# Kernel optimization log

Measured on AMD Instinct MI355X. Metric: run time of the kernel, lower is better.

Reference implementation:

```python
import jax, jax.numpy as jnp
import numpy as np

T, B = 1024, 64
IN, HID, OUT, ASZ = 512, 512, 512, 128


def lstm_cell(x, h, c, Wih, Whh, bih, bhh):
    g = x @ Wih.T + bih + h @ Whh.T + bhh
    i, f, gg, o = jnp.split(g, 4, axis=1)
    c2 = jax.nn.sigmoid(f) * c + jax.nn.sigmoid(i) * jnp.tanh(gg)
    h2 = jax.nn.sigmoid(o) * jnp.tanh(c2)
    return h2, c2


def arnn_cell(x, h, pol, Wih, Whh, b, ninp, nhid):
    # policy chunks: [ninp, nhid, nhid, nhid, nhid, nhid]
    p_in = pol[:, :ninp]
    p_h = pol[:, ninp:ninp + nhid]
    p_ig = pol[:, ninp + nhid:ninp + 2 * nhid]
    p_hg = pol[:, ninp + 2 * nhid:ninp + 3 * nhid]
    p_b = pol[:, ninp + 3 * nhid:ninp + 4 * nhid]
    ig = ((x * p_in) @ Wih.T) * p_ig + b * p_b
    hg = ((h * p_h) @ Whh.T) * p_hg
    return jnp.tanh(ig + hg)


def setup_inputs() -> dict:
    key = jax.random.key(0)
    ks = list(jax.random.split(key, 24))
    s = 0.1
    d = {"x": jax.random.normal(ks[0], (T, B, IN), dtype=jnp.float32)}
    # layer 0: ninp=IN, nhid=HID; layer 1: ninp=HID, nhid=OUT
    for l, (ninp, nhid) in enumerate([(IN, HID), (HID, OUT)]):
        ain = ASZ + ninp + nhid
        psz = ninp + 5 * nhid
        base = 1 + 9 * l
        d[f"aW_ih{l}"] = jax.random.normal(ks[base + 0], (4 * ASZ, ain)) * s
        d[f"aW_hh{l}"] = jax.random.normal(ks[base + 1], (4 * ASZ, ASZ)) * s
        d[f"ab_ih{l}"] = jax.random.normal(ks[base + 2], (4 * ASZ,)) * s
        d[f"ab_hh{l}"] = jax.random.normal(ks[base + 3], (4 * ASZ,)) * s
        d[f"pW{l}"] = jax.random.normal(ks[base + 4], (psz, ASZ)) * s
        d[f"pb{l}"] = jax.random.normal(ks[base + 5], (psz,)) * s
        d[f"fW_ih{l}"] = jax.random.normal(ks[base + 6], (nhid, ninp)) * s
        d[f"fW_hh{l}"] = jax.random.normal(ks[base + 7], (nhid, nhid)) * s
        d[f"fb{l}"] = jax.random.normal(ks[base + 8], (nhid,)) * s
    return d


def reference(x, aW_ih0, aW_hh0, ab_ih0, ab_hh0, pW0, pb0, fW_ih0, fW_hh0, fb0,
              aW_ih1, aW_hh1, ab_ih1, ab_hh1, pW1, pb1, fW_ih1, fW_hh1, fb1):
    zB = lambda n: jnp.zeros((B, n), dtype=x.dtype)
    init = (zB(ASZ), zB(ASZ), zB(ASZ), zB(ASZ), zB(HID), zB(OUT))

    def step(carry, xt):
        ahx0, ahc0, ahx1, ahc1, fhx0, fhx1 = carry
        # layer 0: adapt input = [x_t, fhx0, adapt_hx of layer -1 (= layer 1)]
        ax0 = jnp.concatenate([xt, fhx0, ahx1], axis=1)
        ahx0, ahc0 = lstm_cell(ax0, ahx0, ahc0, aW_ih0, aW_hh0, ab_ih0, ab_hh0)
        pol0 = ahx0 @ pW0.T + pb0
        fhx0 = arnn_cell(xt, fhx0, pol0, fW_ih0, fW_hh0, fb0, IN, HID)
        # layer 1
        ax1 = jnp.concatenate([fhx0, fhx1, ahx0], axis=1)
        ahx1, ahc1 = lstm_cell(ax1, ahx1, ahc1, aW_ih1, aW_hh1, ab_ih1, ab_hh1)
        pol1 = ahx1 @ pW1.T + pb1
        fhx1 = arnn_cell(fhx0, fhx1, pol1, fW_ih1, fW_hh1, fb1, HID, OUT)
        return (ahx0, ahc0, ahx1, ahc1, fhx0, fhx1), fhx1

    _, out = jax.lax.scan(step, init, x)  # out: [T, B, OUT]
    return out
```

## Files before the change

### kernel.cpp

```cpp
#include <hip/hip_runtime.h>

#define TT    1024
#define NTHR  512
#define NWG   256

#define XB_SZ  65536
#define XA0    0
#define XA1    2048
#define XF0    4096
#define XF1    12288
#define XP0    20480
#define XP1    40960
#define X_ZERO_END 20480

#define O_BARB (8 * XB_SZ)

__device__ __forceinline__ float sigm(float x) { return 1.f / (1.f + __expf(-x)); }

__device__ __forceinline__ float dot_ks(const float* __restrict__ a,
                                        const float* __restrict__ w,
                                        int nq, int ks) {
  float s0=0.f,s1=0.f,s2=0.f,s3=0.f;
  const float4* a4=(const float4*)a; const float4* w4=(const float4*)w;
  #pragma unroll 8
  for (int k = 0; k < nq; ++k) {
    int i4 = (k<<2) + ks;
    float4 av = a4[i4], wv = w4[i4];
    s0=fmaf(av.x,wv.x,s0); s1=fmaf(av.y,wv.y,s1);
    s2=fmaf(av.z,wv.z,s2); s3=fmaf(av.w,wv.w,s3);
  }
  return (s0+s1)+(s2+s3);
}
__device__ __forceinline__ float dot3_ks(const float* __restrict__ a,
                                         const float* __restrict__ pp,
                                         const float* __restrict__ w,
                                         int nq, int ks) {
  float s0=0.f,s1=0.f,s2=0.f,s3=0.f;
  const float4* a4=(const float4*)a; const float4* p4=(const float4*)pp;
  const float4* w4=(const float4*)w;
  #pragma unroll 8
  for (int k = 0; k < nq; ++k) {
    int i4 = (k<<2) + ks;
    float4 av = a4[i4], pv = p4[i4], wv = w4[i4];
    s0=fmaf(av.x*pv.x,wv.x,s0); s1=fmaf(av.y*pv.y,wv.y,s1);
    s2=fmaf(av.z*pv.z,wv.z,s2); s3=fmaf(av.w*pv.w,wv.w,s3);
  }
  return (s0+s1)+(s2+s3);
}
__device__ __forceinline__ float dot_full(const float* __restrict__ a,
                                          const float* __restrict__ w) {
  float s0=0.f,s1=0.f,s2=0.f,s3=0.f;
  const float4* a4=(const float4*)a; const float4* w4=(const float4*)w;
  #pragma unroll 8
  for (int k = 0; k < 32; ++k) {
    float4 av = a4[k], wv = w4[k];
    s0=fmaf(av.x,wv.x,s0); s1=fmaf(av.y,wv.y,s1);
    s2=fmaf(av.z,wv.z,s2); s3=fmaf(av.w,wv.w,s3);
  }
  return (s0+s1)+(s2+s3);
}

__device__ __forceinline__ void xbar(int* cnt, int* ep, int e, int tid) {
  __syncthreads();
  if (tid == 0) {
    int old = __hip_atomic_fetch_add(cnt, 1, __ATOMIC_RELAXED,
                                     __HIP_MEMORY_SCOPE_AGENT);
    if (old == e * 32 - 1)
      __hip_atomic_store(ep, e, __ATOMIC_RELAXED, __HIP_MEMORY_SCOPE_AGENT);
    while (__hip_atomic_load(ep, __ATOMIC_RELAXED,
                             __HIP_MEMORY_SCOPE_AGENT) < e)
      __builtin_amdgcn_s_sleep(1);
    (void)__hip_atomic_load(ep, __ATOMIC_ACQUIRE, __HIP_MEMORY_SCOPE_AGENT);
  }
  __syncthreads();
}

struct Params {
  const float* x;
  const float *aW_ih0, *aW_hh0, *ab_ih0, *ab_hh0, *pW0, *pb0, *fW_ih0, *fW_hh0, *fb0;
  const float *aW_ih1, *aW_hh1, *ab_ih1, *ab_hh1, *pW1, *pb1, *fW_ih1, *fW_hh1, *fb1;
  float* out;
  float* ws;
};

__global__ __launch_bounds__(NTHR, 1)
void arnn_kernel(Params p) {
  extern __shared__ float lds[];
  __shared__ int s_rank;
  const int tid = threadIdx.x;
  float* __restrict__ ws = p.ws;

  int xcd;
  asm volatile("s_getreg_b32 %0, hwreg(HW_REG_XCC_ID)" : "=s"(xcd));
  xcd &= 7;

  int* bar = (int*)(ws + O_BARB);
  if (tid == 0)
    s_rank = __hip_atomic_fetch_add(&bar[2048 + xcd], 1,
                                    __ATOMIC_RELAXED, __HIP_MEMORY_SCOPE_AGENT);
  __syncthreads();
  const int r = s_rank;
  int* cnt = &bar[xcd * 256];
  int* ep  = &bar[xcd * 256 + 64];

  float* xb = ws + (size_t)xcd * XB_SZ;
  const int b0 = xcd * 8;

  for (int i = r * NTHR + tid; i < X_ZERO_END; i += 32 * NTHR) xb[i] = 0.f;

  const int lane = tid & 63;
  const int ks   = tid & 3;
  const int jj = tid >> 7, blL = (tid >> 4) & 7, q = (tid >> 2) & 3;
  const int jL = r * 4 + jj;
  const bool cell = (tid & 15) == 0;
  const int c4 = tid >> 5, blA = (tid >> 2) & 7;
  const int cA = r * 16 + c4;
  const int nA = r * 80 + (tid >> 3), blP = tid & 7;
  const int nB = r * 80 + 64 + (tid >> 3);

  float bi0=0,bf0=0,bg0=0,bo0=0, bi1=0,bf1=0,bg1=0,bo1=0;
  if (cell) {
    bi0 = p.ab_ih0[0*128+jL] + p.ab_hh0[0*128+jL];
    bf0 = p.ab_ih0[1*128+jL] + p.ab_hh0[1*128+jL];
    bg0 = p.ab_ih0[2*128+jL] + p.ab_hh0[2*128+jL];
    bo0 = p.ab_ih0[3*128+jL] + p.ab_hh0[3*128+jL];
    bi1 = p.ab_ih1[0*128+jL] + p.ab_hh1[0*128+jL];
    bf1 = p.ab_ih1[1*128+jL] + p.ab_hh1[1*128+jL];
    bg1 = p.ab_ih1[2*128+jL] + p.ab_hh1[2*128+jL];
    bo1 = p.ab_ih1[3*128+jL] + p.ab_hh1[3*128+jL];
  }
  const float fb0c = p.fb0[cA], fb1c = p.fb1[cA];
  const float pb0a = p.pb0[nA], pb1a = p.pb1[nA];
  float pb0b = 0.f, pb1b = 0.f;
  if (tid < 128) { pb0b = p.pb0[nB]; pb1b = p.pb1[nB]; }

  const int rowL = q * 128 + jL;
  const float* wih0 = p.aW_ih0 + (size_t)rowL * 1152;
  const float* whh0 = p.aW_hh0 + (size_t)rowL * 128;
  const float* wih1 = p.aW_ih1 + (size_t)rowL * 1152;
  const float* whh1 = p.aW_hh1 + (size_t)rowL * 128;
  const float* fwi0 = p.fW_ih0 + (size_t)cA * 512;
  const float* fwh0 = p.fW_hh0 + (size_t)cA * 512;
  const float* fwi1 = p.fW_ih1 + (size_t)cA * 512;
  const float* fwh1 = p.fW_hh1 + (size_t)cA * 512;

  float creg0 = 0.f, creg1 = 0.f;

  int e = 1;
  xbar(cnt, ep, e, tid);

  for (int t = 0; t < TT; ++t) {
    const int old = t & 1, nw = old ^ 1;
    float* ahx0_o = xb + XA0 + old * 1024;
    float* ahx0_n = xb + XA0 + nw  * 1024;
    float* ahx1_o = xb + XA1 + old * 1024;
    float* ahx1_n = xb + XA1 + nw  * 1024;
    float* fhx0_o = xb + XF0 + old * 4096;
    float* fhx0_n = xb + XF0 + nw  * 4096;
    float* fhx1_o = xb + XF1 + old * 4096;
    float* fhx1_n = xb + XF1 + nw  * 4096;
    float* pol0   = xb + XP0;
    float* pol1   = xb + XP1;
    const float* xt = p.x + ((size_t)t * 64 + b0) * 512;

    {
      float s = dot_ks(xt     + blL * 512, wih0,        32, ks)
              + dot_ks(fhx0_o + blL * 512, wih0 + 512,  32, ks)
              + dot_ks(ahx1_o + blL * 128, wih0 + 1024,  8, ks)
              + dot_ks(ahx0_o + blL * 128, whh0,         8, ks);
      s += __shfl_xor(s, 1); s += __shfl_xor(s, 2);
      float gi = __shfl(s,(lane&48)+0),  gf = __shfl(s,(lane&48)+4);
      float gg = __shfl(s,(lane&48)+8),  go = __shfl(s,(lane&48)+12);
      if (cell) {
        gi += bi0; gf += bf0; gg += bg0; go += bo0;
        float c2 = sigm(gf) * creg0 + sigm(gi) * tanhf(gg);
        creg0 = c2;
        ahx0_n[blL * 128 + jL] = sigm(go) * tanhf(c2);
      }
    }
    ++e; xbar(cnt, ep, e, tid);

    {
      pol0[blP * 2560 + nA] = pb0a +
          dot_full(ahx0_n + blP * 128, p.pW0 + (size_t)nA * 128);
      if (tid < 128)
        pol0[blP * 2560 + nB] = pb0b +
            dot_full(ahx0_n + blP * 128, p.pW0 + (size_t)nB * 128);
    }
    ++e; xbar(cnt, ep, e, tid);

    {
      const float* pr = pol0 + blA * 2560;
      float sig = dot3_ks(xt     + blA * 512, pr,       fwi0, 32, ks);
      float shg = dot3_ks(fhx0_o + blA * 512, pr + 512, fwh0, 32, ks);
      sig += __shfl_xor(sig, 1); sig += __shfl_xor(sig, 2);
      shg += __shfl_xor(shg, 1); shg += __shfl_xor(shg, 2);
      if (ks == 0) {
        float v = tanhf(sig * pr[1024 + cA] + fb0c * pr[2048 + cA]
                      + shg * pr[1536 + cA]);
        fhx0_n[blA * 512 + cA] = v;
      }
    }
    ++e; xbar(cnt, ep, e, tid);

    {
      float s = dot_ks(fhx0_n + blL * 512, wih1,        32, ks)
              + dot_ks(fhx1_o + blL * 512, wih1 + 512,  32, ks)
              + dot_ks(ahx0_n + blL * 128, wih1 + 1024,  8, ks)
              + dot_ks(ahx1_o + blL * 128, whh1,         8, ks);
      s += __shfl_xor(s, 1); s += __shfl_xor(s, 2);
      float gi = __shfl(s,(lane&48)+0),  gf = __shfl(s,(lane&48)+4);
      float gg = __shfl(s,(lane&48)+8),  go = __shfl(s,(lane&48)+12);
      if (cell) {
        gi += bi1; gf += bf1; gg += bg1; go += bo1;
        float c2 = sigm(gf) * creg1 + sigm(gi) * tanhf(gg);
        creg1 = c2;
        ahx1_n[blL * 128 + jL] = sigm(go) * tanhf(c2);
      }
    }
    ++e; xbar(cnt, ep, e, tid);

    {
      pol1[blP * 2560 + nA] = pb1a +
          dot_full(ahx1_n + blP * 128, p.pW1 + (size_t)nA * 128);
      if (tid < 128)
        pol1[blP * 2560 + nB] = pb1b +
            dot_full(ahx1_n + blP * 128, p.pW1 + (size_t)nB * 128);
    }
    ++e; xbar(cnt, ep, e, tid);

    {
      const float* pr = pol1 + blA * 2560;
      float sig = dot3_ks(fhx0_n + blA * 512, pr,       fwi1, 32, ks);
      float shg = dot3_ks(fhx1_o + blA * 512, pr + 512, fwh1, 32, ks);
      sig += __shfl_xor(sig, 1); sig += __shfl_xor(sig, 2);
      shg += __shfl_xor(shg, 1); shg += __shfl_xor(shg, 2);
      if (ks == 0) {
        float v = tanhf(sig * pr[1024 + cA] + fb1c * pr[2048 + cA]
                      + shg * pr[1536 + cA]);
        fhx1_n[blA * 512 + cA] = v;
        p.out[((size_t)t * 64 + b0 + blA) * 512 + cA] = v;
      }
    }
    ++e; xbar(cnt, ep, e, tid);
  }
  (void)lds;
}

extern "C" void kernel_launch(void* const* d_in, const int* in_sizes, int n_in,
                              void* d_out, int out_size, void* d_ws, size_t ws_size,
                              hipStream_t stream) {
  Params prm;
  prm.x      = (const float*)d_in[0];
  prm.aW_ih0 = (const float*)d_in[1];
  prm.aW_hh0 = (const float*)d_in[2];
  prm.ab_ih0 = (const float*)d_in[3];
  prm.ab_hh0 = (const float*)d_in[4];
  prm.pW0    = (const float*)d_in[5];
  prm.pb0    = (const float*)d_in[6];
  prm.fW_ih0 = (const float*)d_in[7];
  prm.fW_hh0 = (const float*)d_in[8];
  prm.fb0    = (const float*)d_in[9];
  prm.aW_ih1 = (const float*)d_in[10];
  prm.aW_hh1 = (const float*)d_in[11];
  prm.ab_ih1 = (const float*)d_in[12];
  prm.ab_hh1 = (const float*)d_in[13];
  prm.pW1    = (const float*)d_in[14];
  prm.pb1    = (const float*)d_in[15];
  prm.fW_ih1 = (const float*)d_in[16];
  prm.fW_hh1 = (const float*)d_in[17];
  prm.fb1    = (const float*)d_in[18];
  prm.out    = (float*)d_out;
  prm.ws     = (float*)d_ws;

  hipMemsetAsync((char*)d_ws + (size_t)O_BARB * 4, 0, 16384, stream);

  static int lds_bytes = 84 * 1024;
  hipFuncSetAttribute((const void*)arnn_kernel,
                      hipFuncAttributeMaxDynamicSharedMemorySize, lds_bytes);

  void* kargs[] = { (void*)&prm };
  hipLaunchCooperativeKernel((const void*)arnn_kernel, dim3(NWG), dim3(NTHR),
                             kargs, lds_bytes, stream);
}
```

Measured before the change: 98.07 ms.

## Cache LSTM input weights in LDS and double threads per workgroup

Each workgroup now preloads its 16 rows of aW_ih0 and aW_ih1 into shared memory (about 147 KB) once, so the per-step LSTM gate dot products read weights from LDS instead of global/L2 memory. The thread count per workgroup doubles to 1024, with eight-way K splits and a three-level shuffle reduction, so each thread's dot product is shorter. Barrier atomics move to acquire-release ordering. The risks are higher LDS pressure, a launch_bounds value of 4 that does not match one 1024-thread block per CU, and larger workgroups making __syncthreads costlier.

```diff
diff --git a/kernel.cpp b/kernel.cpp
--- a/kernel.cpp
+++ b/kernel.cpp
@@ -1,7 +1,7 @@
 #include <hip/hip_runtime.h>
 
 #define TT    1024
-#define NTHR  512
+#define NTHR  1024
 #define NWG   256
 
 #define XB_SZ  65536
@@ -17,30 +17,30 @@
 
 __device__ __forceinline__ float sigm(float x) { return 1.f / (1.f + __expf(-x)); }
 
-__device__ __forceinline__ float dot_ks(const float* __restrict__ a,
-                                        const float* __restrict__ w,
-                                        int nq, int ks) {
+__device__ __forceinline__ float dot8(const float* __restrict__ a,
+                                      const float* __restrict__ w,
+                                      int nq, int ks) {
   float s0=0.f,s1=0.f,s2=0.f,s3=0.f;
   const float4* a4=(const float4*)a; const float4* w4=(const float4*)w;
   #pragma unroll 8
   for (int k = 0; k < nq; ++k) {
-    int i4 = (k<<2) + ks;
+    int i4 = (k<<3) + ks;
     float4 av = a4[i4], wv = w4[i4];
     s0=fmaf(av.x,wv.x,s0); s1=fmaf(av.y,wv.y,s1);
     s2=fmaf(av.z,wv.z,s2); s3=fmaf(av.w,wv.w,s3);
   }
   return (s0+s1)+(s2+s3);
 }
-__device__ __forceinline__ float dot3_ks(const float* __restrict__ a,
-                                         const float* __restrict__ pp,
-                                         const float* __restrict__ w,
-                                         int nq, int ks) {
+__device__ __forceinline__ float dot3_8(const float* __restrict__ a,
+                                        const float* __restrict__ pp,
+                                        const float* __restrict__ w,
+                                        int nq, int ks) {
   float s0=0.f,s1=0.f,s2=0.f,s3=0.f;
   const float4* a4=(const float4*)a; const float4* p4=(const float4*)pp;
   const float4* w4=(const float4*)w;
   #pragma unroll 8
   for (int k = 0; k < nq; ++k) {
-    int i4 = (k<<2) + ks;
+    int i4 = (k<<3) + ks;
     float4 av = a4[i4], pv = p4[i4], wv = w4[i4];
     s0=fmaf(av.x*pv.x,wv.x,s0); s1=fmaf(av.y*pv.y,wv.y,s1);
     s2=fmaf(av.z*pv.z,wv.z,s2); s3=fmaf(av.w*pv.w,wv.w,s3);
@@ -63,10 +63,10 @@
 __device__ __forceinline__ void xbar(int* cnt, int* ep, int e, int tid) {
   __syncthreads();
   if (tid == 0) {
-    int old = __hip_atomic_fetch_add(cnt, 1, __ATOMIC_RELAXED,
+    int old = __hip_atomic_fetch_add(cnt, 1, __ATOMIC_ACQ_REL,
                                      __HIP_MEMORY_SCOPE_AGENT);
     if (old == e * 32 - 1)
-      __hip_atomic_store(ep, e, __ATOMIC_RELAXED, __HIP_MEMORY_SCOPE_AGENT);
+      __hip_atomic_store(ep, e, __ATOMIC_RELEASE, __HIP_MEMORY_SCOPE_AGENT);
     while (__hip_atomic_load(ep, __ATOMIC_RELAXED,
                              __HIP_MEMORY_SCOPE_AGENT) < e)
       __builtin_amdgcn_s_sleep(1);
@@ -83,7 +83,7 @@
   float* ws;
 };
 
-__global__ __launch_bounds__(NTHR, 1)
+__global__ __launch_bounds__(NTHR, 4)
 void arnn_kernel(Params p) {
   extern __shared__ float lds[];
   __shared__ int s_rank;
@@ -106,17 +106,30 @@
   float* xb = ws + (size_t)xcd * XB_SZ;
   const int b0 = xcd * 8;
 
+  {
+    const float4* g0 = (const float4*)p.aW_ih0;
+    const float4* g1 = (const float4*)p.aW_ih1;
+    float4* l0 = (float4*)lds;
+    float4* l1 = (float4*)(lds + 16 * 1152);
+    for (int i4 = tid; i4 < 4608; i4 += NTHR) {
+      int rr = i4 / 288, c = i4 - rr * 288;
+      int q = rr >> 2, jj = rr & 3;
+      size_t grow = (size_t)(q * 128 + r * 4 + jj) * 288;
+      l0[rr * 288 + c] = g0[grow + c];
+      l1[rr * 288 + c] = g1[grow + c];
+    }
+  }
   for (int i = r * NTHR + tid; i < X_ZERO_END; i += 32 * NTHR) xb[i] = 0.f;
 
   const int lane = tid & 63;
-  const int ks   = tid & 3;
-  const int jj = tid >> 7, blL = (tid >> 4) & 7, q = (tid >> 2) & 3;
+  const int ksL = tid & 7, q = (tid >> 3) & 3, blL = (tid >> 5) & 7, jj = (tid >> 8) & 3;
   const int jL = r * 4 + jj;
-  const bool cell = (tid & 15) == 0;
-  const int c4 = tid >> 5, blA = (tid >> 2) & 7;
+  const bool cell = (tid & 31) == 0;
+  const int ksA = tid & 7, blA = (tid >> 3) & 7, c4 = (tid >> 6) & 15;
   const int cA = r * 16 + c4;
-  const int nA = r * 80 + (tid >> 3), blP = tid & 7;
-  const int nB = r * 80 + 64 + (tid >> 3);
+  const int nAr = tid >> 3, blP = tid & 7;
+  const bool polt = tid < 640;
+  const int nA = r * 80 + nAr;
 
   float bi0=0,bf0=0,bg0=0,bo0=0, bi1=0,bf1=0,bg1=0,bo1=0;
   if (cell) {
@@ -130,19 +143,19 @@
     bo1 = p.ab_ih1[3*128+jL] + p.ab_hh1[3*128+jL];
   }
   const float fb0c = p.fb0[cA], fb1c = p.fb1[cA];
-  const float pb0a = p.pb0[nA], pb1a = p.pb1[nA];
-  float pb0b = 0.f, pb1b = 0.f;
-  if (tid < 128) { pb0b = p.pb0[nB]; pb1b = p.pb1[nB]; }
+  float pb0a = 0.f, pb1a = 0.f;
+  if (polt) { pb0a = p.pb0[nA]; pb1a = p.pb1[nA]; }
 
   const int rowL = q * 128 + jL;
-  const float* wih0 = p.aW_ih0 + (size_t)rowL * 1152;
   const float* whh0 = p.aW_hh0 + (size_t)rowL * 128;
-  const float* wih1 = p.aW_ih1 + (size_t)rowL * 1152;
   const float* whh1 = p.aW_hh1 + (size_t)rowL * 128;
   const float* fwi0 = p.fW_ih0 + (size_t)cA * 512;
   const float* fwh0 = p.fW_hh0 + (size_t)cA * 512;
   const float* fwi1 = p.fW_ih1 + (size_t)cA * 512;
   const float* fwh1 = p.fW_hh1 + (size_t)cA * 512;
+
+  const float* wL0 = lds + (q * 4 + jj) * 1152;
+  const float* wL1 = lds + 16 * 1152 + (q * 4 + jj) * 1152;
 
   float creg0 = 0.f, creg1 = 0.f;
 
@@ -164,13 +177,13 @@
     const float* xt = p.x + ((size_t)t * 64 + b0) * 512;
 
     {
-      float s = dot_ks(xt     + blL * 512, wih0,        32, ks)
-              + dot_ks(fhx0_o + blL * 512, wih0 + 512,  32, ks)
-              + dot_ks(ahx1_o + blL * 128, wih0 + 1024,  8, ks)
-              + dot_ks(ahx0_o + blL * 128, whh0,         8, ks);
-      s += __shfl_xor(s, 1); s += __shfl_xor(s, 2);
-      float gi = __shfl(s,(lane&48)+0),  gf = __shfl(s,(lane&48)+4);
-      float gg = __shfl(s,(lane&48)+8),  go = __shfl(s,(lane&48)+12);
+      float s = dot8(xt     + blL * 512, wL0,        16, ksL)
+              + dot8(fhx0_o + blL * 512, wL0 + 512,  16, ksL)
+              + dot8(ahx1_o + blL * 128, wL0 + 1024,  4, ksL)
+              + dot8(ahx0_o + blL * 128, whh0,        4, ksL);
+      s += __shfl_xor(s, 1); s += __shfl_xor(s, 2); s += __shfl_xor(s, 4);
+      float gi = __shfl(s,(lane&32)+0),  gf = __shfl(s,(lane&32)+8);
+      float gg = __shfl(s,(lane&32)+16), go = __shfl(s,(lane&32)+24);
       if (cell) {
         gi += bi0; gf += bf0; gg += bg0; go += bo0;
         float c2 = sigm(gf) * creg0 + sigm(gi) * tanhf(gg);
@@ -180,22 +193,19 @@
     }
     ++e; xbar(cnt, ep, e, tid);
 
-    {
+    if (polt) {
       pol0[blP * 2560 + nA] = pb0a +
           dot_full(ahx0_n + blP * 128, p.pW0 + (size_t)nA * 128);
-      if (tid < 128)
-        pol0[blP * 2560 + nB] = pb0b +
-            dot_full(ahx0_n + blP * 128, p.pW0 + (size_t)nB * 128);
     }
     ++e; xbar(cnt, ep, e, tid);
 
     {
       const float* pr = pol0 + blA * 2560;
-      float sig = dot3_ks(xt     + blA * 512, pr,       fwi0, 32, ks);
-      float shg = dot3_ks(fhx0_o + blA * 512, pr + 512, fwh0, 32, ks);
-      sig += __shfl_xor(sig, 1); sig += __shfl_xor(sig, 2);
-      shg += __shfl_xor(shg, 1); shg += __shfl_xor(shg, 2);
-      if (ks == 0) {
+      float sig = dot3_8(xt     + blA * 512, pr,       fwi0, 16, ksA);
+      float shg = dot3_8(fhx0_o + blA * 512, pr + 512, fwh0, 16, ksA);
+      sig += __shfl_xor(sig, 1); sig += __shfl_xor(sig, 2); sig += __shfl_xor(sig, 4);
+      shg += __shfl_xor(shg, 1); shg += __shfl_xor(shg, 2); shg += __shfl_xor(shg, 4);
+      if (ksA == 0) {
         float v = tanhf(sig * pr[1024 + cA] + fb0c * pr[2048 + cA]
                       + shg * pr[1536 + cA]);
         fhx0_n[blA * 512 + cA] = v;
@@ -204,13 +214,13 @@
     ++e; xbar(cnt, ep, e, tid);
 
     {
-      float s = dot_ks(fhx0_n + blL * 512, wih1,        32, ks)
-              + dot_ks(fhx1_o + blL * 512, wih1 + 512,  32, ks)
-              + dot_ks(ahx0_n + blL * 128, wih1 + 1024,  8, ks)
-              + dot_ks(ahx1_o + blL * 128, whh1,         8, ks);
-      s += __shfl_xor(s, 1); s += __shfl_xor(s, 2);
-      float gi = __shfl(s,(lane&48)+0),  gf = __shfl(s,(lane&48)+4);
-      float gg = __shfl(s,(lane&48)+8),  go = __shfl(s,(lane&48)+12);
+      float s = dot8(fhx0_n + blL * 512, wL1,        16, ksL)
+              + dot8(fhx1_o + blL * 512, wL1 + 512,  16, ksL)
+              + dot8(ahx0_n + blL * 128, wL1 + 1024,  4, ksL)
+              + dot8(ahx1_o + blL * 128, whh1,        4, ksL);
+      s += __shfl_xor(s, 1); s += __shfl_xor(s, 2); s += __shfl_xor(s, 4);
+      float gi = __shfl(s,(lane&32)+0),  gf = __shfl(s,(lane&32)+8);
+      float gg = __shfl(s,(lane&32)+16), go = __shfl(s,(lane&32)+24);
       if (cell) {
         gi += bi1; gf += bf1; gg += bg1; go += bo1;
         float c2 = sigm(gf) * creg1 + sigm(gi) * tanhf(gg);
@@ -220,22 +230,19 @@
     }
     ++e; xbar(cnt, ep, e, tid);
 
-    {
+    if (polt) {
       pol1[blP * 2560 + nA] = pb1a +
           dot_full(ahx1_n + blP * 128, p.pW1 + (size_t)nA * 128);
-      if (tid < 128)
-        pol1[blP * 2560 + nB] = pb1b +
-            dot_full(ahx1_n + blP * 128, p.pW1 + (size_t)nB * 128);
     }
     ++e; xbar(cnt, ep, e, tid);
 
     {
       const float* pr = pol1 + blA * 2560;
-      float sig = dot3_ks(fhx0_n + blA * 512, pr,       fwi1, 32, ks);
-      float shg = dot3_ks(fhx1_o + blA * 512, pr + 512, fwh1, 32, ks);
-      sig += __shfl_xor(sig, 1); sig += __shfl_xor(sig, 2);
-      shg += __shfl_xor(shg, 1); shg += __shfl_xor(shg, 2);
-      if (ks == 0) {
+      float sig = dot3_8(fhx0_n + blA * 512, pr,       fwi1, 16, ksA);
+      float shg = dot3_8(fhx1_o + blA * 512, pr + 512, fwh1, 16, ksA);
+      sig += __shfl_xor(sig, 1); sig += __shfl_xor(sig, 2); sig += __shfl_xor(sig, 4);
+      shg += __shfl_xor(shg, 1); shg += __shfl_xor(shg, 2); shg += __shfl_xor(shg, 4);
+      if (ksA == 0) {
         float v = tanhf(sig * pr[1024 + cA] + fb1c * pr[2048 + cA]
                       + shg * pr[1536 + cA]);
         fhx1_n[blA * 512 + cA] = v;
@@ -244,7 +251,6 @@
     }
     ++e; xbar(cnt, ep, e, tid);
   }
-  (void)lds;
 }
 
 extern "C" void kernel_launch(void* const* d_in, const int* in_sizes, int n_in,
@@ -275,7 +281,7 @@
 
   hipMemsetAsync((char*)d_ws + (size_t)O_BARB * 4, 0, 16384, stream);
 
-  static int lds_bytes = 84 * 1024;
+  static int lds_bytes = 2 * 16 * 1152 * 4;
   hipFuncSetAttribute((const void*)arnn_kernel,
                       hipFuncAttributeMaxDynamicSharedMemorySize, lds_bytes);
 
```

Result: slower. 134.7 ms (+37.4%).

## Stage shared recurrent state and policy into LDS once per phase

Applied to the files above, without the earlier changes.

Before each phase, every workgroup cooperatively copies the hidden states and policy vectors it reads from global workspace into padded LDS buffers, using relaxed agent-scope atomic loads, then runs the dot products from LDS. This replaces many repeated, possibly uncached global reads of data written by other workgroups with one coalesced copy per phase. It also drops the acquire load from the grid barrier and relies on the atomic loads for visibility instead. The cost is an extra __syncthreads and the copy work per phase, plus a risk to memory-ordering correctness.

```diff
diff --git a/kernel.cpp b/kernel.cpp
--- a/kernel.cpp
+++ b/kernel.cpp
@@ -15,7 +15,29 @@
 
 #define O_BARB (8 * XB_SZ)
 
+#define L_F0O  0
+#define L_F0N  4160
+#define L_F1O  8320
+#define L_A1O  12480
+#define L_A0O  13568
+#define L_A0N  14656
+#define L_A1N  15744
+#define L_POL  16832
+#define LDS_F  37376
+
 __device__ __forceinline__ float sigm(float x) { return 1.f / (1.f + __expf(-x)); }
+
+template <int RW2, int LS2>
+__device__ __forceinline__ void stage_r(const float* g, float* l, int rows, int tid) {
+  const unsigned long long* gs = (const unsigned long long*)g;
+  unsigned long long* ls = (unsigned long long*)l;
+  const int tot = rows * RW2;
+  for (int i = tid; i < tot; i += NTHR) {
+    int rr = i / RW2, cc = i - rr * RW2;
+    ls[rr * LS2 + cc] = __hip_atomic_load(&gs[i], __ATOMIC_RELAXED,
+                                          __HIP_MEMORY_SCOPE_AGENT);
+  }
+}
 
 __device__ __forceinline__ float dot_ks(const float* __restrict__ a,
                                         const float* __restrict__ w,
@@ -70,7 +92,6 @@
     while (__hip_atomic_load(ep, __ATOMIC_RELAXED,
                              __HIP_MEMORY_SCOPE_AGENT) < e)
       __builtin_amdgcn_s_sleep(1);
-    (void)__hip_atomic_load(ep, __ATOMIC_ACQUIRE, __HIP_MEMORY_SCOPE_AGENT);
   }
   __syncthreads();
 }
@@ -115,8 +136,9 @@
   const bool cell = (tid & 15) == 0;
   const int c4 = tid >> 5, blA = (tid >> 2) & 7;
   const int cA = r * 16 + c4;
-  const int nA = r * 80 + (tid >> 3), blP = tid & 7;
-  const int nB = r * 80 + 64 + (tid >> 3);
+  const int nAr = tid >> 3, blP = tid & 7;
+  const int nA = r * 80 + nAr;
+  const int nB = r * 80 + 64 + nAr;
 
   float bi0=0,bf0=0,bg0=0,bo0=0, bi1=0,bf1=0,bg1=0,bo1=0;
   if (cell) {
@@ -163,11 +185,15 @@
     float* pol1   = xb + XP1;
     const float* xt = p.x + ((size_t)t * 64 + b0) * 512;
 
-    {
-      float s = dot_ks(xt     + blL * 512, wih0,        32, ks)
-              + dot_ks(fhx0_o + blL * 512, wih0 + 512,  32, ks)
-              + dot_ks(ahx1_o + blL * 128, wih0 + 1024,  8, ks)
-              + dot_ks(ahx0_o + blL * 128, whh0,         8, ks);
+    stage_r<256,260>(fhx0_o, lds + L_F0O, 8, tid);
+    stage_r<64,68>  (ahx1_o, lds + L_A1O, 8, tid);
+    stage_r<64,68>  (ahx0_o, lds + L_A0O, 8, tid);
+    __syncthreads();
+    {
+      float s = dot_ks(xt + blL * 512,          wih0,        32, ks)
+              + dot_ks(lds + L_F0O + blL * 520, wih0 + 512,  32, ks)
+              + dot_ks(lds + L_A1O + blL * 136, wih0 + 1024,  8, ks)
+              + dot_ks(lds + L_A0O + blL * 136, whh0,         8, ks);
       s += __shfl_xor(s, 1); s += __shfl_xor(s, 2);
       float gi = __shfl(s,(lane&48)+0),  gf = __shfl(s,(lane&48)+4);
       float gg = __shfl(s,(lane&48)+8),  go = __shfl(s,(lane&48)+12);
@@ -180,34 +206,41 @@
     }
     ++e; xbar(cnt, ep, e, tid);
 
+    stage_r<64,68>(ahx0_n, lds + L_A0N, 8, tid);
+    __syncthreads();
     {
       pol0[blP * 2560 + nA] = pb0a +
-          dot_full(ahx0_n + blP * 128, p.pW0 + (size_t)nA * 128);
+          dot_full(lds + L_A0N + blP * 136, p.pW0 + (size_t)nA * 128);
       if (tid < 128)
         pol0[blP * 2560 + nB] = pb0b +
-            dot_full(ahx0_n + blP * 128, p.pW0 + (size_t)nB * 128);
-    }
-    ++e; xbar(cnt, ep, e, tid);
-
-    {
-      const float* pr = pol0 + blA * 2560;
-      float sig = dot3_ks(xt     + blA * 512, pr,       fwi0, 32, ks);
-      float shg = dot3_ks(fhx0_o + blA * 512, pr + 512, fwh0, 32, ks);
+            dot_full(lds + L_A0N + blP * 136, p.pW0 + (size_t)nB * 128);
+    }
+    ++e; xbar(cnt, ep, e, tid);
+
+    stage_r<1280,1284>(pol0, lds + L_POL, 8, tid);
+    __syncthreads();
+    {
+      const float* prl = lds + L_POL + blA * 2568;
+      float sig = dot3_ks(xt + blA * 512,          prl,       fwi0, 32, ks);
+      float shg = dot3_ks(lds + L_F0O + blA * 520, prl + 512, fwh0, 32, ks);
       sig += __shfl_xor(sig, 1); sig += __shfl_xor(sig, 2);
       shg += __shfl_xor(shg, 1); shg += __shfl_xor(shg, 2);
       if (ks == 0) {
-        float v = tanhf(sig * pr[1024 + cA] + fb0c * pr[2048 + cA]
-                      + shg * pr[1536 + cA]);
+        float v = tanhf(sig * prl[1024 + cA] + fb0c * prl[2048 + cA]
+                      + shg * prl[1536 + cA]);
         fhx0_n[blA * 512 + cA] = v;
       }
     }
     ++e; xbar(cnt, ep, e, tid);
 
-    {
-      float s = dot_ks(fhx0_n + blL * 512, wih1,        32, ks)
-              + dot_ks(fhx1_o + blL * 512, wih1 + 512,  32, ks)
-              + dot_ks(ahx0_n + blL * 128, wih1 + 1024,  8, ks)
-              + dot_ks(ahx1_o + blL * 128, whh1,         8, ks);
+    stage_r<256,260>(fhx0_n, lds + L_F0N, 8, tid);
+    stage_r<256,260>(fhx1_o, lds + L_F1O, 8, tid);
+    __syncthreads();
+    {
+      float s = dot_ks(lds + L_F0N + blL * 520, wih1,        32, ks)
+              + dot_ks(lds + L_F1O + blL * 520, wih1 + 512,  32, ks)
+              + dot_ks(lds + L_A0N + blL * 136, wih1 + 1024,  8, ks)
+              + dot_ks(lds + L_A1O + blL * 136, whh1,         8, ks);
       s += __shfl_xor(s, 1); s += __shfl_xor(s, 2);
       float gi = __shfl(s,(lane&48)+0),  gf = __shfl(s,(lane&48)+4);
       float gg = __shfl(s,(lane&48)+8),  go = __shfl(s,(lane&48)+12);
@@ -220,31 +253,34 @@
     }
     ++e; xbar(cnt, ep, e, tid);
 
+    stage_r<64,68>(ahx1_n, lds + L_A1N, 8, tid);
+    __syncthreads();
     {
       pol1[blP * 2560 + nA] = pb1a +
-          dot_full(ahx1_n + blP * 128, p.pW1 + (size_t)nA * 128);
+          dot_full(lds + L_A1N + blP * 136, p.pW1 + (size_t)nA * 128);
       if (tid < 128)
         pol1[blP * 2560 + nB] = pb1b +
-            dot_full(ahx1_n + blP * 128, p.pW1 + (size_t)nB * 128);
-    }
-    ++e; xbar(cnt, ep, e, tid);
-
-    {
-      const float* pr = pol1 + blA * 2560;
-      float sig = dot3_ks(fhx0_n + blA * 512, pr,       fwi1, 32, ks);
-      float shg = dot3_ks(fhx1_o + blA * 512, pr + 512, fwh1, 32, ks);
+            dot_full(lds + L_A1N + blP * 136, p.pW1 + (size_t)nB * 128);
+    }
+    ++e; xbar(cnt, ep, e, tid);
+
+    stage_r<1280,1284>(pol1, lds + L_POL, 8, tid);
+    __syncthreads();
+    {
+      const float* prl = lds + L_POL + blA * 2568;
+      float sig = dot3_ks(lds + L_F0N + blA * 520, prl,       fwi1, 32, ks);
+      float shg = dot3_ks(lds + L_F1O + blA * 520, prl + 512, fwh1, 32, ks);
       sig += __shfl_xor(sig, 1); sig += __shfl_xor(sig, 2);
       shg += __shfl_xor(shg, 1); shg += __shfl_xor(shg, 2);
       if (ks == 0) {
-        float v = tanhf(sig * pr[1024 + cA] + fb1c * pr[2048 + cA]
-                      + shg * pr[1536 + cA]);
+        float v = tanhf(sig * prl[1024 + cA] + fb1c * prl[2048 + cA]
+                      + shg * prl[1536 + cA]);
         fhx1_n[blA * 512 + cA] = v;
         p.out[((size_t)t * 64 + b0 + blA) * 512 + cA] = v;
       }
     }
     ++e; xbar(cnt, ep, e, tid);
   }
-  (void)lds;
 }
 
 extern "C" void kernel_launch(void* const* d_in, const int* in_sizes, int n_in,
@@ -275,7 +311,7 @@
 
   hipMemsetAsync((char*)d_ws + (size_t)O_BARB * 4, 0, 16384, stream);
 
-  static int lds_bytes = 84 * 1024;
+  static int lds_bytes = LDS_F * 4;
   hipFuncSetAttribute((const void*)arnn_kernel,
                       hipFuncAttributeMaxDynamicSharedMemorySize, lds_bytes);
 
```

Result: slower. 129.5 ms (+32.1%).
